# Kernel optimization log

Hardware: AMD Instinct MI355X
Metric: run time of the kernel (lower is better)

Reference implementation:

```python
import jax, jax.numpy as jnp
import numpy as np

B, T, E = 8, 1024, 1024
H, HS = 16, 64  # num_heads, head_size; H*HS == E


def setup_inputs() -> dict:
    key = jax.random.key(0)
    k1, k2, k3, k4, k5, k6 = jax.random.split(key, 6)
    x = jax.random.normal(k1, (B, T, E), dtype=jnp.float32)
    s = E ** -0.5
    Wk = jax.random.normal(k2, (H, HS, E), dtype=jnp.float32) * s
    Wq = jax.random.normal(k3, (H, HS, E), dtype=jnp.float32) * s
    Wv = jax.random.normal(k4, (H, HS, E), dtype=jnp.float32) * s
    Wproj = jax.random.normal(k5, (E, E), dtype=jnp.float32) * s
    i = 0
    return {"x": x, "Wk": Wk, "Wq": Wq, "Wv": Wv, "Wproj": Wproj, "i": i}


def reference(x, Wk, Wq, Wv, Wproj, i):
    # choices fixed at full supernet config: embed_dim=E, head_size=HS, no biases.
    b, t, e = x.shape
    hs = Wk.shape[1]
    # per-head projections, heads batched: [B,H,T,HS]
    k = jnp.einsum('bte,hde->bhtd', x, Wk)
    q = jnp.einsum('bte,hde->bhtd', x, Wq)
    v = jnp.einsum('bte,hde->bhtd', x, Wv)
    wei = jnp.einsum('bhtd,bhsd->bhts', q, k) * (hs ** -0.5)  # [B,H,T,T]
    causal = jnp.tril(jnp.ones((t, t), dtype=bool))
    wei = jnp.where(causal, wei, -jnp.inf)
    wei = jax.nn.softmax(wei, axis=-1)  # dropout p=0 (eval)
    out = jnp.einsum('bhts,bhsd->bthd', wei, v).reshape(b, t, -1)  # concat heads
    out = out @ Wproj.T  # proj, bias_proj=False
    return out
```

## Files before the change

### kernel.cpp

```cpp
#include <hip/hip_runtime.h>

#define B_  8
#define T_  1024
#define E_  1024
#define H_  16
#define HS_ 64
#define K_  1024

typedef __bf16 bf16x8 __attribute__((ext_vector_type(8)));
typedef __bf16 bf16x4 __attribute__((ext_vector_type(4)));
typedef float  f32x4  __attribute__((ext_vector_type(4)));
typedef unsigned short us;

__device__ __forceinline__ us f2bf(float f) {
    union { float f; unsigned int i; } c; c.f = f;
    unsigned int x = c.i;
    return (us)((x + 0x7fff + ((x >> 16) & 1)) >> 16);
}
__device__ __forceinline__ us f2bf_t(float f) {
    union { float f; unsigned int i; } c; c.f = f;
    return (us)(c.i >> 16);
}
__device__ __forceinline__ bf16x8 cvt8(const float* p) {
    float4 a = *reinterpret_cast<const float4*>(p);
    float4 b = *reinterpret_cast<const float4*>(p + 4);
    union { bf16x8 v; us u[8]; } c;
    c.u[0] = f2bf(a.x); c.u[1] = f2bf(a.y); c.u[2] = f2bf(a.z); c.u[3] = f2bf(a.w);
    c.u[4] = f2bf(b.x); c.u[5] = f2bf(b.y); c.u[6] = f2bf(b.z); c.u[7] = f2bf(b.w);
    return c.v;
}
__device__ __forceinline__ void async_cp16(const us* g, us* l) {
    __builtin_amdgcn_global_load_lds((const unsigned int*)g, (unsigned int*)l, 16, 0, 0);
}

__device__ __forceinline__ f32x4 mfma_pv16(bf16x4 a, bf16x4 b, f32x4 c) {
#if __has_builtin(__builtin_amdgcn_mfma_f32_16x16x16_bf16)
    return __builtin_amdgcn_mfma_f32_16x16x16_bf16(a, b, c, 0, 0, 0);
#elif __has_builtin(__builtin_amdgcn_mfma_f32_16x16x16bf16_1k)
    typedef short s16x4 __attribute__((ext_vector_type(4)));
    union U { bf16x4 b; s16x4 s; };
    U ua, ub; ua.b = a; ub.b = b;
    return __builtin_amdgcn_mfma_f32_16x16x16bf16_1k(ua.s, ub.s, c, 0, 0, 0);
#else
    f32x4 d = c;
    asm("v_mfma_f32_16x16x16_bf16 %0, %1, %2, %0" : "+v"(d) : "v"(a), "v"(b));
    return d;
#endif
}

__global__ __launch_bounds__(256) void cvt_kernel(
    const float* __restrict__ sx, const float* __restrict__ sq,
    const float* __restrict__ sk, const float* __restrict__ sv,
    const float* __restrict__ sp,
    us* __restrict__ dx, us* __restrict__ dq, us* __restrict__ dk,
    us* __restrict__ dv, us* __restrict__ dp)
{
    const int y = blockIdx.y;
    const float* src = (y == 0) ? sx : (y == 1) ? sq : (y == 2) ? sk : (y == 3) ? sv : sp;
    us*          dst = (y == 0) ? dx : (y == 1) ? dq : (y == 2) ? dk : (y == 3) ? dv : dp;
    const size_t n = (y == 0) ? (size_t)B_ * T_ * E_ : (size_t)E_ * E_;
    const size_t i = ((size_t)blockIdx.x * 256 + threadIdx.x) * 8;
    if (i >= n) return;
    *reinterpret_cast<bf16x8*>(dst + i) = cvt8(src + i);
}

__global__ __launch_bounds__(256) void qkv_gf(
    const us* __restrict__ A,
    const us* __restrict__ Wq, const us* __restrict__ Wk, const us* __restrict__ Wv,
    us* __restrict__ q, us* __restrict__ k, us* __restrict__ vT)
{
    const int type = blockIdx.z;
    const us* Bm = (type == 0) ? Wq : (type == 1) ? Wk : Wv;
    us* out      = (type == 0) ? q  : (type == 1) ? k  : vT;
    const int vtrans = (type == 2);

    __shared__ __align__(16) us As[128 * 64];
    __shared__ __align__(16) us Bs[128 * 64];

    const int tid  = threadIdx.x;
    const int lane = tid & 63;
    const int w    = tid >> 6;
    const int quad = lane >> 4;
    const int l15  = lane & 15;
    const int wm   = w >> 1, wn = w & 1;
    const int row0 = blockIdx.x * 128;
    const int col0 = blockIdx.y * 128;
    const int x7   = l15 & 7;
    const int ca0  = (quad ^ x7) * 8;
    const int ca1  = ((4 + quad) ^ x7) * 8;

    const us* pa[4]; const us* pb[4];
#pragma unroll
    for (int i = 0; i < 4; ++i) {
        const int idx = tid + i * 256;
        const int r   = idx >> 3;
        const int c8  = ((idx & 7) ^ (r & 7)) * 8;
        pa[i] = A  + (size_t)(row0 + r) * K_ + c8;
        pb[i] = Bm + (size_t)(col0 + r) * K_ + c8;
    }

    f32x4 acc[4][4] = {};
    for (int k0 = 0; k0 < K_; k0 += 64) {
        __syncthreads();
#pragma unroll
        for (int i = 0; i < 4; ++i) {
            async_cp16(pa[i], &As[(tid + i * 256) * 8]);
            async_cp16(pb[i], &Bs[(tid + i * 256) * 8]);
            pa[i] += 64; pb[i] += 64;
        }
        __syncthreads();
#pragma unroll
        for (int kk = 0; kk < 2; ++kk) {
            const int ca = kk ? ca1 : ca0;
            bf16x8 af[4], bf[4];
#pragma unroll
            for (int t = 0; t < 4; ++t) {
                af[t] = *reinterpret_cast<const bf16x8*>(&As[(wm * 64 + t * 16 + l15) * 64 + ca]);
                bf[t] = *reinterpret_cast<const bf16x8*>(&Bs[(wn * 64 + t * 16 + l15) * 64 + ca]);
            }
#pragma unroll
            for (int mt = 0; mt < 4; ++mt)
#pragma unroll
                for (int nt = 0; nt < 4; ++nt)
                    acc[mt][nt] = __builtin_amdgcn_mfma_f32_16x16x32_bf16(af[mt], bf[nt], acc[mt][nt], 0, 0, 0);
        }
    }

#pragma unroll
    for (int mt = 0; mt < 4; ++mt)
#pragma unroll
        for (int nt = 0; nt < 4; ++nt)
#pragma unroll
            for (int r = 0; r < 4; ++r) {
                const int m = row0 + wm * 64 + mt * 16 + quad * 4 + r;
                const int n = col0 + wn * 64 + nt * 16 + l15;
                const int b = m >> 10, t = m & 1023;
                const int h = n >> 6,  d = n & 63;
                const us vb = f2bf(acc[mt][nt][r]);
                if (vtrans)  out[((size_t)((b * 16 + h) * 64 + d)) * 1024 + t] = vb;
                else         out[((size_t)(b * 16 + h) * 1024 + t) * 64 + d] = vb;
            }
}

__global__ __launch_bounds__(256) void proj_gf(
    const us* __restrict__ A, const us* __restrict__ Bm, float* __restrict__ C)
{
    __shared__ __align__(16) us As[128 * 64];
    __shared__ __align__(16) us Bs[128 * 64];

    const int tid  = threadIdx.x;
    const int lane = tid & 63;
    const int w    = tid >> 6;
    const int quad = lane >> 4;
    const int l15  = lane & 15;
    const int wm   = w >> 1, wn = w & 1;
    const int row0 = blockIdx.x * 128;
    const int col0 = blockIdx.y * 128;
    const int x7   = l15 & 7;
    const int ca0  = (quad ^ x7) * 8;
    const int ca1  = ((4 + quad) ^ x7) * 8;

    const us* pa[4]; const us* pb[4];
#pragma unroll
    for (int i = 0; i < 4; ++i) {
        const int idx = tid + i * 256;
        const int r   = idx >> 3;
        const int c8  = ((idx & 7) ^ (r & 7)) * 8;
        pa[i] = A  + (size_t)(row0 + r) * K_ + c8;
        pb[i] = Bm + (size_t)(col0 + r) * K_ + c8;
    }

    f32x4 acc[4][4] = {};
    for (int k0 = 0; k0 < K_; k0 += 64) {
        __syncthreads();
#pragma unroll
        for (int i = 0; i < 4; ++i) {
            async_cp16(pa[i], &As[(tid + i * 256) * 8]);
            async_cp16(pb[i], &Bs[(tid + i * 256) * 8]);
            pa[i] += 64; pb[i] += 64;
        }
        __syncthreads();
#pragma unroll
        for (int kk = 0; kk < 2; ++kk) {
            const int ca = kk ? ca1 : ca0;
            bf16x8 af[4], bf[4];
#pragma unroll
            for (int t = 0; t < 4; ++t) {
                af[t] = *reinterpret_cast<const bf16x8*>(&As[(wm * 64 + t * 16 + l15) * 64 + ca]);
                bf[t] = *reinterpret_cast<const bf16x8*>(&Bs[(wn * 64 + t * 16 + l15) * 64 + ca]);
            }
#pragma unroll
            for (int mt = 0; mt < 4; ++mt)
#pragma unroll
                for (int nt = 0; nt < 4; ++nt)
                    acc[mt][nt] = __builtin_amdgcn_mfma_f32_16x16x32_bf16(af[mt], bf[nt], acc[mt][nt], 0, 0, 0);
        }
    }

#pragma unroll
    for (int mt = 0; mt < 4; ++mt)
#pragma unroll
        for (int nt = 0; nt < 4; ++nt)
#pragma unroll
            for (int r = 0; r < 4; ++r) {
                const int m = row0 + wm * 64 + mt * 16 + quad * 4 + r;
                const int n = col0 + wn * 64 + nt * 16 + l15;
                C[(size_t)m * E_ + n] = acc[mt][nt][r];
            }
}

#define CSCALE 0.18033688011112042f

__global__ __launch_bounds__(256) void attn_v9(
    const us* __restrict__ Q, const us* __restrict__ K,
    const us* __restrict__ VT, us* __restrict__ O)
{
    const int px = blockIdx.x;
    const int bh = blockIdx.y;
    const int tA = px, tB = 15 - px;
    const size_t base  = (size_t)bh * T_ * HS_;
    const size_t baseT = (size_t)bh * HS_ * T_;
    const int tid  = threadIdx.x;
    const int w    = tid >> 6;
    const int lane = tid & 63;
    const int quad = lane >> 4;
    const int l15  = lane & 15;

    __shared__ __align__(16) us kt[64][72];
    __shared__ __align__(16) us vt[64][72];

    const int rowA = tA * 64 + w * 16;
    const int rowB = tB * 64 + w * 16;

    bf16x8 qfA0, qfA1, qfB0, qfB1;
    {
        const us* qa = Q + base + (size_t)(rowA + l15) * HS_ + quad * 8;
        const us* qb = Q + base + (size_t)(rowB + l15) * HS_ + quad * 8;
        qfA0 = *reinterpret_cast<const bf16x8*>(qa);
        qfA1 = *reinterpret_cast<const bf16x8*>(qa + 32);
        qfB0 = *reinterpret_cast<const bf16x8*>(qb);
        qfB1 = *reinterpret_cast<const bf16x8*>(qb + 32);
    }

    const int sr0 = tid >> 3;
    const int sc0 = (tid & 7) * 8;
    const int sr1 = sr0 + 32;

    const us* kp0 = K + base + (size_t)sr0 * HS_ + sc0;
    const us* kp1 = K + base + (size_t)sr1 * HS_ + sc0;
    const us* vp0 = VT + baseT + (size_t)sr0 * T_ + sc0;
    const us* vp1 = VT + baseT + (size_t)sr1 * T_ + sc0;

    float lA = 0.f, lB = 0.f;
    f32x4 oA[4] = {}, oB[4] = {};

    bf16x8 kr0, kr1, vr0, vr1;
    kr0 = *reinterpret_cast<const bf16x8*>(kp0);
    kr1 = *reinterpret_cast<const bf16x8*>(kp1);
    vr0 = *reinterpret_cast<const bf16x8*>(vp0);
    vr1 = *reinterpret_cast<const bf16x8*>(vp1);

    const int nch = tB + 1;
    for (int ch = 0; ch < nch; ++ch) {
        const int s0 = ch * 64;
        const bool actA = (ch <= tA);

        __syncthreads();
        *reinterpret_cast<bf16x8*>(&kt[sr0][sc0]) = kr0;
        *reinterpret_cast<bf16x8*>(&kt[sr1][sc0]) = kr1;
        *reinterpret_cast<bf16x8*>(&vt[sr0][sc0]) = vr0;
        *reinterpret_cast<bf16x8*>(&vt[sr1][sc0]) = vr1;
        __syncthreads();

        if (ch + 1 < nch) {
            kp0 += 64 * HS_; kp1 += 64 * HS_; vp0 += 64; vp1 += 64;
            kr0 = *reinterpret_cast<const bf16x8*>(kp0);
            kr1 = *reinterpret_cast<const bf16x8*>(kp1);
            vr0 = *reinterpret_cast<const bf16x8*>(vp0);
            vr1 = *reinterpret_cast<const bf16x8*>(vp1);
        }

        f32x4 sA[4] = {}, sB[4] = {};
#pragma unroll
        for (int nt = 0; nt < 4; ++nt) {
            bf16x8 kf0 = *reinterpret_cast<const bf16x8*>(&kt[nt * 16 + l15][quad * 8]);
            bf16x8 kf1 = *reinterpret_cast<const bf16x8*>(&kt[nt * 16 + l15][quad * 8 + 32]);
            sB[nt] = __builtin_amdgcn_mfma_f32_16x16x32_bf16(kf0, qfB0, sB[nt], 0, 0, 0);
            sB[nt] = __builtin_amdgcn_mfma_f32_16x16x32_bf16(kf1, qfB1, sB[nt], 0, 0, 0);
            if (actA) {
                sA[nt] = __builtin_amdgcn_mfma_f32_16x16x32_bf16(kf0, qfA0, sA[nt], 0, 0, 0);
                sA[nt] = __builtin_amdgcn_mfma_f32_16x16x32_bf16(kf1, qfA1, sA[nt], 0, 0, 0);
            }
        }
        if (ch == tB) {
#pragma unroll
            for (int nt = 0; nt < 4; ++nt)
#pragma unroll
                for (int r = 0; r < 4; ++r)
                    if (s0 + nt * 16 + quad * 4 + r > rowB + l15) sB[nt][r] = -1e30f;
        }
        if (ch == tA) {
#pragma unroll
            for (int nt = 0; nt < 4; ++nt)
#pragma unroll
                for (int r = 0; r < 4; ++r)
                    if (s0 + nt * 16 + quad * 4 + r > rowA + l15) sA[nt][r] = -1e30f;
        }

        bf16x4 paB[4], paA[4];
#pragma unroll
        for (int nt = 0; nt < 4; ++nt) {
            union { bf16x4 v; us u[4]; } pk;
#pragma unroll
            for (int r = 0; r < 4; ++r) {
                const float p = exp2f(sB[nt][r] * CSCALE);
                lB += p;
                pk.u[r] = f2bf_t(p);
            }
            paB[nt] = pk.v;
        }
        if (actA) {
#pragma unroll
            for (int nt = 0; nt < 4; ++nt) {
                union { bf16x4 v; us u[4]; } pk;
#pragma unroll
                for (int r = 0; r < 4; ++r) {
                    const float p = exp2f(sA[nt][r] * CSCALE);
                    lA += p;
                    pk.u[r] = f2bf_t(p);
                }
                paA[nt] = pk.v;
            }
        }

#pragma unroll
        for (int dt = 0; dt < 4; ++dt) {
#pragma unroll
            for (int nt = 0; nt < 4; ++nt) {
                const bf16x4 vf = *reinterpret_cast<const bf16x4*>(
                    &vt[dt * 16 + l15][nt * 16 + quad * 4]);
                oB[dt] = mfma_pv16(paB[nt], vf, oB[dt]);
                if (actA) oA[dt] = mfma_pv16(paA[nt], vf, oA[dt]);
            }
        }
    }

    lA += __shfl_xor(lA, 16); lA += __shfl_xor(lA, 32);
    lB += __shfl_xor(lB, 16); lB += __shfl_xor(lB, 32);

    const int b = bh >> 4, h = bh & 15;
#pragma unroll
    for (int r = 0; r < 4; ++r) {
        const int src = (lane & 48) + quad * 4 + r;
        const float invA = 1.f / __shfl(lA, src);
        const float invB = 1.f / __shfl(lB, src);
        const size_t offA = ((size_t)b * T_ + rowA + quad * 4 + r) * E_ + h * HS_;
        const size_t offB = ((size_t)b * T_ + rowB + quad * 4 + r) * E_ + h * HS_;
#pragma unroll
        for (int dt = 0; dt < 4; ++dt) {
            O[offA + dt * 16 + l15] = f2bf(oA[dt][r] * invA);
            O[offB + dt * 16 + l15] = f2bf(oB[dt][r] * invB);
        }
    }
}

extern "C" void kernel_launch(void* const* d_in, const int* in_sizes, int n_in,
                              void* d_out, int out_size, void* d_ws, size_t ws_size,
                              hipStream_t stream) {
    const float* x  = (const float*)d_in[0];
    const float* Wk = (const float*)d_in[1];
    const float* Wq = (const float*)d_in[2];
    const float* Wv = (const float*)d_in[3];
    const float* Wp = (const float*)d_in[4];

    const size_t qe = (size_t)B_ * H_ * T_ * HS_;
    const size_t we = (size_t)E_ * E_;

    us* xb = (us*)d_ws;
    us* wq = xb + qe;
    us* wk = wq + we;
    us* wv = wk + we;
    us* wp = wv + we;
    us* q  = wp + we;
    us* k  = q + qe;
    us* vT = k + qe;
    us* o  = xb;

    cvt_kernel<<<dim3(4096, 5), 256, 0, stream>>>(x, Wq, Wk, Wv, Wp,
                                                  xb, wq, wk, wv, wp);
    qkv_gf<<<dim3(64, 8, 3), 256, 0, stream>>>(xb, wq, wk, wv, q, k, vT);
    attn_v9<<<dim3(8, 128), 256, 0, stream>>>(q, k, vT, o);
    proj_gf<<<dim3(64, 8), 256, 0, stream>>>(o, wp, (float*)d_out);
}
```

Before: 250.8 us.

## Double-buffer attention K/V tiles with async global-to-LDS copies and XOR swizzle

The attention kernel now stages K and V^T chunks into two LDS buffers using async 16-byte global-to-LDS copies. The next chunk is prefetched while the current one is computed, which replaces the register staging and the two barriers per chunk with a single barrier. The padded LDS layout becomes an unpadded one with an XOR swizzle to avoid bank conflicts, and the loop is unrolled by two so the buffer index is a compile-time constant. This doubles LDS use and depends on async_cp16 being defined elsewhere and waited on correctly before the barrier.

```diff
diff --git a/kernel.cpp b/kernel.cpp
--- a/kernel.cpp
+++ b/kernel.cpp
@@ -211,7 +211,84 @@
 
 #define CSCALE 0.18033688011112042f
 
-__global__ __launch_bounds__(256) void attn_v9(
+#define ATT_BODY(P, CH)                                                        \
+    {                                                                          \
+        const int s0 = (CH) * 64;                                              \
+        const bool actA = ((CH) <= tA);                                        \
+        if ((CH) + 1 < nch) {          \
+            async_cp16(kp0, &kt[(P) ^ 1][d0]);                                 \
+            async_cp16(kp1, &kt[(P) ^ 1][d1]);                                 \
+            async_cp16(vp0, &vt[(P) ^ 1][d0]);                                 \
+            async_cp16(vp1, &vt[(P) ^ 1][d1]);                                 \
+            kp0 += 64 * HS_; kp1 += 64 * HS_; vp0 += 64; vp1 += 64;            \
+        }                                                                      \
+        f32x4 sA[4] = {}, sB[4] = {};                                          \
+        _Pragma("unroll")                                                      \
+        for (int nt = 0; nt < 4; ++nt) {                                       \
+            const int krow = (nt * 16 + l15) * 64;                             \
+            bf16x8 kf0 = *reinterpret_cast<const bf16x8*>(&kt[P][krow + ca0]); \
+            bf16x8 kf1 = *reinterpret_cast<const bf16x8*>(&kt[P][krow + ca1]); \
+            sB[nt] = __builtin_amdgcn_mfma_f32_16x16x32_bf16(kf0, qfB0, sB[nt], 0, 0, 0); \
+            sB[nt] = __builtin_amdgcn_mfma_f32_16x16x32_bf16(kf1, qfB1, sB[nt], 0, 0, 0); \
+            if (actA) {                                                        \
+                sA[nt] = __builtin_amdgcn_mfma_f32_16x16x32_bf16(kf0, qfA0, sA[nt], 0, 0, 0); \
+                sA[nt] = __builtin_amdgcn_mfma_f32_16x16x32_bf16(kf1, qfA1, sA[nt], 0, 0, 0); \
+            }                                                                  \
+        }                                                                      \
+        if ((CH) == tB) {                                                      \
+            _Pragma("unroll")                                                  \
+            for (int nt = 0; nt < 4; ++nt)                                     \
+                _Pragma("unroll")                                              \
+                for (int r = 0; r < 4; ++r)                                    \
+                    if (s0 + nt * 16 + quad * 4 + r > rowB + l15) sB[nt][r] = -1e30f; \
+        }                                                                      \
+        if ((CH) == tA) {                                                      \
+            _Pragma("unroll")                                                  \
+            for (int nt = 0; nt < 4; ++nt)                                     \
+                _Pragma("unroll")                                              \
+                for (int r = 0; r < 4; ++r)                                    \
+                    if (s0 + nt * 16 + quad * 4 + r > rowA + l15) sA[nt][r] = -1e30f; \
+        }                                                                      \
+        bf16x4 paB[4], paA[4];                                                 \
+        _Pragma("unroll")                                                      \
+        for (int nt = 0; nt < 4; ++nt) {                                       \
+            union { bf16x4 v; us u[4]; } pk;                                   \
+            _Pragma("unroll")                                                  \
+            for (int r = 0; r < 4; ++r) {                                      \
+                const float p = exp2f(sB[nt][r] * CSCALE);                     \
+                lB += p;                                                       \
+                pk.u[r] = f2bf_t(p);                                           \
+            }                                                                  \
+            paB[nt] = pk.v;                                                    \
+        }                                                                      \
+        if (actA) {                                                            \
+            _Pragma("unroll")                                                  \
+            for (int nt = 0; nt < 4; ++nt) {                                   \
+                union { bf16x4 v; us u[4]; } pk;                               \
+                _Pragma("unroll")                                              \
+                for (int r = 0; r < 4; ++r) {                                  \
+                    const float p = exp2f(sA[nt][r] * CSCALE);                 \
+                    lA += p;                                                   \
+                    pk.u[r] = f2bf_t(p);                                       \
+                }                                                              \
+                paA[nt] = pk.v;                                                \
+            }                                                                  \
+        }                                                                      \
+        _Pragma("unroll")                                                      \
+        for (int dt = 0; dt < 4; ++dt) {                                       \
+            const int vrow = (dt * 16 + l15) * 64;                             \
+            _Pragma("unroll")                                                  \
+            for (int nt = 0; nt < 4; ++nt) {                                   \
+                const int vc = ((2 * nt + (quad >> 1)) ^ x7) * 8 + (quad & 1) * 4; \
+                const bf16x4 vf = *reinterpret_cast<const bf16x4*>(&vt[P][vrow + vc]); \
+                oB[dt] = mfma_pv16(paB[nt], vf, oB[dt]);                       \
+                if (actA) oA[dt] = mfma_pv16(paA[nt], vf, oA[dt]);             \
+            }                                                                  \
+        }                                                                      \
+        __syncthreads();                                                       \
+    }
+
+__global__ __launch_bounds__(256) void attn_v10(
     const us* __restrict__ Q, const us* __restrict__ K,
     const us* __restrict__ VT, us* __restrict__ O)
 {
@@ -221,13 +298,16 @@
     const size_t base  = (size_t)bh * T_ * HS_;
     const size_t baseT = (size_t)bh * HS_ * T_;
     const int tid  = threadIdx.x;
+    const int lane = tid & 63;
     const int w    = tid >> 6;
-    const int lane = tid & 63;
     const int quad = lane >> 4;
     const int l15  = lane & 15;
-
-    __shared__ __align__(16) us kt[64][72];
-    __shared__ __align__(16) us vt[64][72];
+    const int x7   = l15 & 7;
+    const int ca0  = (quad ^ x7) * 8;
+    const int ca1  = ((4 + quad) ^ x7) * 8;
+
+    __shared__ __align__(16) us kt[2][64 * 64];
+    __shared__ __align__(16) us vt[2][64 * 64];
 
     const int rowA = tA * 64 + w * 16;
     const int rowB = tB * 64 + w * 16;
@@ -242,107 +322,28 @@
         qfB1 = *reinterpret_cast<const bf16x8*>(qb + 32);
     }
 
-    const int sr0 = tid >> 3;
-    const int sc0 = (tid & 7) * 8;
-    const int sr1 = sr0 + 32;
-
-    const us* kp0 = K + base + (size_t)sr0 * HS_ + sc0;
-    const us* kp1 = K + base + (size_t)sr1 * HS_ + sc0;
-    const us* vp0 = VT + baseT + (size_t)sr0 * T_ + sc0;
-    const us* vp1 = VT + baseT + (size_t)sr1 * T_ + sc0;
+    const int idx0 = tid, idx1 = tid + 256;
+    const int r0 = idx0 >> 3, r1 = idx1 >> 3;
+    const int d0 = idx0 * 8,  d1 = idx1 * 8;
+    const us* kp0 = K + base + (size_t)r0 * HS_ + ((idx0 & 7) ^ (r0 & 7)) * 8;
+    const us* kp1 = K + base + (size_t)r1 * HS_ + ((idx1 & 7) ^ (r1 & 7)) * 8;
+    const us* vp0 = VT + baseT + (size_t)r0 * T_ + ((idx0 & 7) ^ (r0 & 7)) * 8;
+    const us* vp1 = VT + baseT + (size_t)r1 * T_ + ((idx1 & 7) ^ (r1 & 7)) * 8;
 
     float lA = 0.f, lB = 0.f;
     f32x4 oA[4] = {}, oB[4] = {};
 
-    bf16x8 kr0, kr1, vr0, vr1;
-    kr0 = *reinterpret_cast<const bf16x8*>(kp0);
-    kr1 = *reinterpret_cast<const bf16x8*>(kp1);
-    vr0 = *reinterpret_cast<const bf16x8*>(vp0);
-    vr1 = *reinterpret_cast<const bf16x8*>(vp1);
-
     const int nch = tB + 1;
-    for (int ch = 0; ch < nch; ++ch) {
-        const int s0 = ch * 64;
-        const bool actA = (ch <= tA);
-
-        __syncthreads();
-        *reinterpret_cast<bf16x8*>(&kt[sr0][sc0]) = kr0;
-        *reinterpret_cast<bf16x8*>(&kt[sr1][sc0]) = kr1;
-        *reinterpret_cast<bf16x8*>(&vt[sr0][sc0]) = vr0;
-        *reinterpret_cast<bf16x8*>(&vt[sr1][sc0]) = vr1;
-        __syncthreads();
-
-        if (ch + 1 < nch) {
-            kp0 += 64 * HS_; kp1 += 64 * HS_; vp0 += 64; vp1 += 64;
-            kr0 = *reinterpret_cast<const bf16x8*>(kp0);
-            kr1 = *reinterpret_cast<const bf16x8*>(kp1);
-            vr0 = *reinterpret_cast<const bf16x8*>(vp0);
-            vr1 = *reinterpret_cast<const bf16x8*>(vp1);
-        }
-
-        f32x4 sA[4] = {}, sB[4] = {};
-#pragma unroll
-        for (int nt = 0; nt < 4; ++nt) {
-            bf16x8 kf0 = *reinterpret_cast<const bf16x8*>(&kt[nt * 16 + l15][quad * 8]);
-            bf16x8 kf1 = *reinterpret_cast<const bf16x8*>(&kt[nt * 16 + l15][quad * 8 + 32]);
-            sB[nt] = __builtin_amdgcn_mfma_f32_16x16x32_bf16(kf0, qfB0, sB[nt], 0, 0, 0);
-            sB[nt] = __builtin_amdgcn_mfma_f32_16x16x32_bf16(kf1, qfB1, sB[nt], 0, 0, 0);
-            if (actA) {
-                sA[nt] = __builtin_amdgcn_mfma_f32_16x16x32_bf16(kf0, qfA0, sA[nt], 0, 0, 0);
-                sA[nt] = __builtin_amdgcn_mfma_f32_16x16x32_bf16(kf1, qfA1, sA[nt], 0, 0, 0);
-            }
-        }
-        if (ch == tB) {
-#pragma unroll
-            for (int nt = 0; nt < 4; ++nt)
-#pragma unroll
-                for (int r = 0; r < 4; ++r)
-                    if (s0 + nt * 16 + quad * 4 + r > rowB + l15) sB[nt][r] = -1e30f;
-        }
-        if (ch == tA) {
-#pragma unroll
-            for (int nt = 0; nt < 4; ++nt)
-#pragma unroll
-                for (int r = 0; r < 4; ++r)
-                    if (s0 + nt * 16 + quad * 4 + r > rowA + l15) sA[nt][r] = -1e30f;
-        }
-
-        bf16x4 paB[4], paA[4];
-#pragma unroll
-        for (int nt = 0; nt < 4; ++nt) {
-            union { bf16x4 v; us u[4]; } pk;
-#pragma unroll
-            for (int r = 0; r < 4; ++r) {
-                const float p = exp2f(sB[nt][r] * CSCALE);
-                lB += p;
-                pk.u[r] = f2bf_t(p);
-            }
-            paB[nt] = pk.v;
-        }
-        if (actA) {
-#pragma unroll
-            for (int nt = 0; nt < 4; ++nt) {
-                union { bf16x4 v; us u[4]; } pk;
-#pragma unroll
-                for (int r = 0; r < 4; ++r) {
-                    const float p = exp2f(sA[nt][r] * CSCALE);
-                    lA += p;
-                    pk.u[r] = f2bf_t(p);
-                }
-                paA[nt] = pk.v;
-            }
-        }
-
-#pragma unroll
-        for (int dt = 0; dt < 4; ++dt) {
-#pragma unroll
-            for (int nt = 0; nt < 4; ++nt) {
-                const bf16x4 vf = *reinterpret_cast<const bf16x4*>(
-                    &vt[dt * 16 + l15][nt * 16 + quad * 4]);
-                oB[dt] = mfma_pv16(paB[nt], vf, oB[dt]);
-                if (actA) oA[dt] = mfma_pv16(paA[nt], vf, oA[dt]);
-            }
-        }
+    async_cp16(kp0, &kt[0][d0]);
+    async_cp16(kp1, &kt[0][d1]);
+    async_cp16(vp0, &vt[0][d0]);
+    async_cp16(vp1, &vt[0][d1]);
+    kp0 += 64 * HS_; kp1 += 64 * HS_; vp0 += 64; vp1 += 64;
+    __syncthreads();
+
+    for (int ch = 0; ch < nch; ch += 2) {
+        ATT_BODY(0, ch)
+        if (ch + 1 < nch) ATT_BODY(1, ch + 1)
     }
 
     lA += __shfl_xor(lA, 16); lA += __shfl_xor(lA, 32);
@@ -389,6 +390,6 @@
     cvt_kernel<<<dim3(4096, 5), 256, 0, stream>>>(x, Wq, Wk, Wv, Wp,
                                                   xb, wq, wk, wv, wp);
     qkv_gf<<<dim3(64, 8, 3), 256, 0, stream>>>(xb, wq, wk, wv, q, k, vT);
-    attn_v9<<<dim3(8, 128), 256, 0, stream>>>(q, k, vT, o);
+    attn_v10<<<dim3(8, 128), 256, 0, stream>>>(q, k, vT, o);
     proj_gf<<<dim3(64, 8), 256, 0, stream>>>(o, wp, (float*)d_out);
 }
```

After: 257.7 us. 2.7% more time.
